# Optimization experiments

Measured on AMD Instinct MI355X. Metric: run time of the kernel, lower is better.

Reference implementation:

```python
import jax, jax.numpy as jnp
import numpy as np

B, L0, L1, NS, D, H, NL, HM = 16, 512, 256, 32, 256, 8, 4, 4
T = L0 + L1 + NS + 1
HD = D // H
EPS = 1e-5
SCALE = HD ** -0.5


def setup_inputs() -> dict:
    key = jax.random.key(0)
    ks = jax.random.split(key, 20)
    s = 0.02
    return {
        'seq_tokens_0': jax.random.normal(ks[0], (B, L0, D), jnp.float32),
        'seq_tokens_1': jax.random.normal(ks[1], (B, L1, D), jnp.float32),
        'seq_lens_0': jax.random.randint(ks[2], (B,), 0, L0),
        'seq_lens_1': jax.random.randint(ks[3], (B,), 0, L1),
        'ns_tokens': jax.random.normal(ks[4], (B, NS, D), jnp.float32),
        'domain_emb': jax.random.normal(ks[5], (2, D), jnp.float32) * s,
        'cls_token': jax.random.normal(ks[6], (1, 1, D), jnp.float32) * s,
        'ln1_w': jnp.ones((NL, D), jnp.float32),
        'ln1_b': jnp.zeros((NL, D), jnp.float32),
        'qkv_w': jax.random.normal(ks[7], (NL, D, 3 * D), jnp.float32) * s,
        'qkv_b': jnp.zeros((NL, 3 * D), jnp.float32),
        'out_w': jax.random.normal(ks[8], (NL, D, D), jnp.float32) * s,
        'out_b': jnp.zeros((NL, D), jnp.float32),
        'ln2_w': jnp.ones((NL, D), jnp.float32),
        'ln2_b': jnp.zeros((NL, D), jnp.float32),
        'ffn1_w': jax.random.normal(ks[9], (NL, D, HM * D), jnp.float32) * s,
        'ffn1_b': jnp.zeros((NL, HM * D), jnp.float32),
        'ffn2_w': jax.random.normal(ks[10], (NL, HM * D, D), jnp.float32) * s,
        'ffn2_b': jnp.zeros((NL, D), jnp.float32),
        'fln_w': jnp.ones((D,), jnp.float32),
        'fln_b': jnp.zeros((D,), jnp.float32),
    }


def _ln(x, w, b):
    m = jnp.mean(x, -1, keepdims=True)
    v = jnp.var(x, -1, keepdims=True)
    return (x - m) * jax.lax.rsqrt(v + EPS) * w + b


def _build_mask(seq_lens_0, seq_lens_1):
    # static block structure: intra-domain causal, S<->NS bidirectional, CLS sink row
    base = jnp.zeros((T, T), bool)
    base = base.at[:L0, :L0].set(jnp.tril(jnp.ones((L0, L0), bool)))
    base = base.at[L0:L0 + L1, L0:L0 + L1].set(jnp.tril(jnp.ones((L1, L1), bool)))
    ns_s, ns_e = L0 + L1, L0 + L1 + NS
    base = base.at[:ns_s, ns_s:ns_e].set(True)   # S -> NS
    base = base.at[ns_s:ns_e, :ns_e].set(True)   # NS -> S and NS -> NS
    base = base.at[T - 1, :ns_e].set(True)       # CLS reads all S/NS
    base = base.at[T - 1, T - 1].set(True)       # CLS reads itself
    # per-batch padding mask on keys of each seq segment
    kv = jnp.ones((B, T), bool)
    kv = kv.at[:, :L0].set(jnp.arange(L0)[None, :] < seq_lens_0[:, None])
    kv = kv.at[:, L0:L0 + L1].set(jnp.arange(L1)[None, :] < seq_lens_1[:, None])
    return base[None] & kv[:, None, :]  # [B, T, T]


def _attention(x, mask, qkv_w, qkv_b, out_w, out_b):
    qkv = (x @ qkv_w + qkv_b).reshape(B, T, 3, H, HD)
    q, k, v = qkv[:, :, 0], qkv[:, :, 1], qkv[:, :, 2]
    scores = jnp.einsum('bqhd,bkhd->bhqk', q, k) * SCALE
    m = mask[:, None]  # [B,1,T,T]
    s = jnp.where(m, scores, -jnp.inf)
    any_valid = jnp.any(m, -1, keepdims=True)
    mx = jnp.where(any_valid, jnp.max(s, -1, keepdims=True), 0.0)
    e = jnp.exp(s - mx)  # masked entries exp(-inf)=0
    denom = jnp.sum(e, -1, keepdims=True)
    probs = e / jnp.maximum(denom, 1e-30)  # fully-masked rows -> zeros
    out = jnp.einsum('bhqk,bkhd->bqhd', probs, v).reshape(B, T, D)
    return out @ out_w + out_b


def reference(seq_tokens_0, seq_tokens_1, seq_lens_0, seq_lens_1, ns_tokens,
              domain_emb, cls_token, ln1_w, ln1_b, qkv_w, qkv_b, out_w, out_b,
              ln2_w, ln2_b, ffn1_w, ffn1_b, ffn2_w, ffn2_b, fln_w, fln_b):
    t0 = seq_tokens_0 + domain_emb[0][None, None, :]
    t1 = seq_tokens_1 + domain_emb[1][None, None, :]
    cls = jnp.broadcast_to(cls_token, (B, 1, D))
    x = jnp.concatenate([t0, t1, ns_tokens, cls], axis=1)  # [B,T,D]
    mask = _build_mask(seq_lens_0, seq_lens_1)
    for l in range(NL):
        x = x + _attention(_ln(x, ln1_w[l], ln1_b[l]), mask,
                           qkv_w[l], qkv_b[l], out_w[l], out_b[l])
        h = _ln(x, ln2_w[l], ln2_b[l])
        h = jax.nn.gelu(h @ ffn1_w[l] + ffn1_b[l], approximate=False)
        x = x + h @ ffn2_w[l] + ffn2_b[l]
    x = _ln(x, fln_w, fln_b)
    return x[:, -1, :]  # CLS state [B,D]
```

## Files before the change

kernel.cpp:

```cpp
#include <hip/hip_runtime.h>
#include <hip/hip_bf16.h>
#include <math.h>

typedef __attribute__((ext_vector_type(8))) unsigned short ushort8;
typedef __attribute__((ext_vector_type(8))) short short8;
typedef __attribute__((ext_vector_type(4))) float f32x4;
typedef __attribute__((ext_vector_type(4))) unsigned short ushort4v;
typedef __attribute__((ext_vector_type(4))) int i32x4;
typedef unsigned int u32;

namespace {
constexpr int B = 16, L0 = 512, L1 = 256, NS = 32, D = 256, H = 8, NL = 4, HM = 4;
constexpr int T = L0 + L1 + NS + 1;
constexpr int HD = D / H;
constexpr int NS_S = L0 + L1;
constexpr int TPAD = 832;
constexpr int ROWP = 13312;
constexpr float EPS = 1e-5f;
constexpr float SCL2  = 0.17677669529663687f * 1.4426950408889634f;
}

__device__ __forceinline__ ushort f2bf(float f) {
    union { float f; unsigned u; } v; v.f = f;
    return (ushort)((v.u + 0x7fffu + ((v.u >> 16) & 1u)) >> 16);
}

__device__ __forceinline__ u32 cvtpk(float a, float b) {
    u32 r;
    asm("v_cvt_pk_bf16_f32 %0, %1, %2" : "=v"(r) : "v"(a), "v"(b));
    return r;
}

__device__ __forceinline__ void gload_lds16(const void* g, void* l) {
    __builtin_amdgcn_global_load_lds(
        (const __attribute__((address_space(1))) u32*)g,
        (__attribute__((address_space(3))) u32*)l, 16, 0, 0);
}

__global__ __launch_bounds__(256) void k_idx(
    const int* __restrict__ len0, const int* __restrict__ len1,
    int* __restrict__ offs, int* __restrict__ rowinfo)
{
    __shared__ int so[17];
    const int tid = threadIdx.x;
    if (tid == 0) {
        int acc = 0;
        for (int b = 0; b < 16; ++b) {
            so[b] = acc;
            const int nv = len0[b] + len1[b] + 33;
            acc += ((nv + 63) >> 6) << 6;
        }
        so[16] = acc;
    }
    __syncthreads();
    if (tid < 17) offs[tid] = so[tid];
    for (int r = tid; r < ROWP; r += 256) {
        int info = -1;
        if (r < so[16]) {
            int b = 15;
            for (int j = 0; j < 15; ++j) if (r < so[j + 1]) { b = j; break; }
            const int loc = r - so[b];
            const int n0 = len0[b], n1 = len1[b];
            if (loc < n0 + n1 + 33) {
                const int t = (loc < n0) ? loc
                            : (loc < n0 + n1) ? (L0 + loc - n0)
                            : (NS_S + loc - n0 - n1);
                info = (b << 16) | t;
            }
        }
        rowinfo[r] = info;
    }
}

__global__ __launch_bounds__(256) void k_wprep_all(
    const float* __restrict__ qkvw, const float* __restrict__ outw,
    const float* __restrict__ f1w, const float* __restrict__ f2w,
    ushort* __restrict__ qkvt, ushort* __restrict__ outt,
    ushort* __restrict__ f1t, ushort* __restrict__ f2t)
{
    int id = blockIdx.x;
    const float* src; ushort* dst; int K, N;
    if (id < 768)        { src = qkvw; dst = qkvt; K = 256;  N = 768;  }
    else if (id < 1024)  { id -= 768;  src = outw; dst = outt; K = 256; N = 256; }
    else if (id < 2048)  { id -= 1024; src = f1w;  dst = f1t;  K = 256; N = 1024; }
    else                 { id -= 2048; src = f2w;  dst = f2t;  K = 1024; N = 256; }
    const int ktiles = K >> 5, per = ktiles * (N >> 5);
    const int layer = id / per, rem = id % per;
    const int kb = (rem % ktiles) * 32, nb = (rem / ktiles) * 32;
    src += (size_t)layer * K * N; dst += (size_t)layer * K * N;

    __shared__ float t[32][33];
    const int c = threadIdx.x & 31, r8 = threadIdx.x >> 5;
#pragma unroll
    for (int rr = 0; rr < 32; rr += 8)
        t[r8 + rr][c] = src[(size_t)(kb + r8 + rr) * N + nb + c];
    __syncthreads();
#pragma unroll
    for (int rr = 0; rr < 32; rr += 8)
        dst[(size_t)(nb + r8 + rr) * K + kb + c] = f2bf(t[c][r8 + rr]);
}

__global__ __launch_bounds__(256) void k_build_ln(
    const float* __restrict__ s0, const float* __restrict__ s1,
    const float* __restrict__ ns, const float* __restrict__ dom,
    const float* __restrict__ cls, const float* __restrict__ lnw,
    const float* __restrict__ lnb, const int* __restrict__ rowinfo,
    float* __restrict__ x, ushort* __restrict__ xn)
{
    const int wid = threadIdx.x >> 6, lane = threadIdx.x & 63;
    const int row = blockIdx.x * 4 + wid;
    if (row >= ROWP) return;
    const int d0 = lane * 4;
    const int info = rowinfo[row];
    if (info < 0) {
        float4 z = {0.f, 0.f, 0.f, 0.f};
        *(float4*)(x + (size_t)row * D + d0) = z;
        ushort4v z4 = {0, 0, 0, 0};
        *(ushort4v*)(xn + (size_t)row * D + d0) = z4;
        return;
    }
    const int b = info >> 16, t = info & 0xFFFF;
    float4 v;
    if (t < L0) {
        v = *(const float4*)(s0 + ((size_t)b * L0 + t) * D + d0);
        float4 dm = *(const float4*)(dom + d0);
        v.x += dm.x; v.y += dm.y; v.z += dm.z; v.w += dm.w;
    } else if (t < NS_S) {
        v = *(const float4*)(s1 + ((size_t)b * L1 + (t - L0)) * D + d0);
        float4 dm = *(const float4*)(dom + D + d0);
        v.x += dm.x; v.y += dm.y; v.z += dm.z; v.w += dm.w;
    } else if (t < NS_S + NS) {
        v = *(const float4*)(ns + ((size_t)b * NS + (t - NS_S)) * D + d0);
    } else {
        v = *(const float4*)(cls + d0);
    }
    *(float4*)(x + (size_t)row * D + d0) = v;
    float s  = v.x + v.y + v.z + v.w;
    float ss = v.x * v.x + v.y * v.y + v.z * v.z + v.w * v.w;
#pragma unroll
    for (int o = 32; o; o >>= 1) { s += __shfl_xor(s, o); ss += __shfl_xor(ss, o); }
    const float mean = s * (1.f / D);
    const float var  = ss * (1.f / D) - mean * mean;
    const float r = rsqrtf(var + EPS);
    float4 wv = *(const float4*)(lnw + d0);
    float4 bv = *(const float4*)(lnb + d0);
    ushort4v o4;
    o4[0] = f2bf((v.x - mean) * r * wv.x + bv.x);
    o4[1] = f2bf((v.y - mean) * r * wv.y + bv.y);
    o4[2] = f2bf((v.z - mean) * r * wv.z + bv.z);
    o4[3] = f2bf((v.w - mean) * r * wv.w + bv.w);
    *(ushort4v*)(xn + (size_t)row * D + d0) = o4;
}

template<bool GELU, bool OBF, bool CLSW>
__global__ __launch_bounds__(256) void k_gemm_mfma(
    const ushort* __restrict__ A, const ushort* __restrict__ Wt,
    const float* __restrict__ bias, void* __restrict__ Cout,
    const int* __restrict__ offs, const int* __restrict__ len0,
    const int* __restrict__ len1, int N, int K, int nOff)
{
    __shared__ ushort As[2][128 * 64];
    __shared__ ushort Bs[2][128 * 64];
    const int tid = threadIdx.x;
    const int lane = tid & 63, w = tid >> 6;
    const int lo = lane & 15, g = lane >> 4;
    const int wr = w >> 1, wc = w & 1;
    int m0;
    if (CLSW) {
        const int bb = blockIdx.x;
        const int clsrow = offs[bb] + len0[bb] + len1[bb] + 32;
        m0 = (clsrow >> 7) << 7;
    } else {
        m0 = blockIdx.x * 128;
        if (m0 >= offs[16]) return;
    }
    const int n0 = (blockIdx.y + nOff) * 128;

    f32x4 zero = {0.f, 0.f, 0.f, 0.f};
    f32x4 acc[4][4];
#pragma unroll
    for (int mi = 0; mi < 4; ++mi)
#pragma unroll
        for (int ni = 0; ni < 4; ++ni) acc[mi][ni] = zero;

    const ushort* srcA[4];
    const ushort* srcB[4];
    int ldsOff[4];
#pragma unroll
    for (int i = 0; i < 4; ++i) {
        const int idx16 = (w * 4 + i) * 64 + lane;
        const int row = idx16 >> 3;
        const int scb = ((idx16 & 7) * 16) ^ ((row & 7) << 4);
        srcA[i] = A  + (size_t)(m0 + row) * K + (scb >> 1);
        srcB[i] = Wt + (size_t)(n0 + row) * K + (scb >> 1);
        ldsOff[i] = (w * 4 + i) * 512;
    }

    const int NT = K >> 6;
#pragma unroll
    for (int i = 0; i < 4; ++i) {
        gload_lds16(srcA[i], &As[0][ldsOff[i]]);
        gload_lds16(srcB[i], &Bs[0][ldsOff[i]]);
    }
    asm volatile("s_waitcnt vmcnt(0)");
    __syncthreads();

    for (int t = 0; t < NT; ++t) {
        const int buf = t & 1;
        if (t + 1 < NT) {
            const int nb = buf ^ 1, ko = (t + 1) * 64;
#pragma unroll
            for (int i = 0; i < 4; ++i) {
                gload_lds16(srcA[i] + ko, &As[nb][ldsOff[i]]);
                gload_lds16(srcB[i] + ko, &Bs[nb][ldsOff[i]]);
            }
        }
#pragma unroll
        for (int kk = 0; kk < 2; ++kk) {
            const int kb = (kk * 64 + g * 16) ^ ((lo & 7) << 4);
            short8 af[4], bfr[4];
#pragma unroll
            for (int mi = 0; mi < 4; ++mi)
                af[mi] = *(const short8*)&As[buf][(wr * 64 + mi * 16 + lo) * 64 + (kb >> 1)];
#pragma unroll
            for (int ni = 0; ni < 4; ++ni)
                bfr[ni] = *(const short8*)&Bs[buf][(wc * 64 + ni * 16 + lo) * 64 + (kb >> 1)];
#pragma unroll
            for (int mi = 0; mi < 4; ++mi)
#pragma unroll
                for (int ni = 0; ni < 4; ++ni)
                    acc[mi][ni] = __builtin_amdgcn_mfma_f32_16x16x32_bf16(
                        af[mi], bfr[ni], acc[mi][ni], 0, 0, 0);
        }
        asm volatile("s_waitcnt vmcnt(0)");
        __syncthreads();
    }

    float bv[4];
#pragma unroll
    for (int ni = 0; ni < 4; ++ni) bv[ni] = bias[n0 + wc * 64 + ni * 16 + lo];
#pragma unroll
    for (int mi = 0; mi < 4; ++mi) {
#pragma unroll
        for (int i = 0; i < 4; ++i) {
            const int row = m0 + wr * 64 + mi * 16 + g * 4 + i;
#pragma unroll
            for (int ni = 0; ni < 4; ++ni) {
                const int col = n0 + wc * 64 + ni * 16 + lo;
                float v = acc[mi][ni][i] + bv[ni];
                if (GELU) v = 0.5f * v * (1.0f + erff(v * 0.70710678118654752f));
                if (OBF) ((ushort*)Cout)[(size_t)row * N + col] = f2bf(v);
                else     ((float*)Cout)[(size_t)row * N + col] = v;
            }
        }
    }
}

template<int MODE, bool CLSW>
__global__ __launch_bounds__(256) void k_gemm_fused(
    const ushort* __restrict__ A, const ushort* __restrict__ Wt,
    const float* __restrict__ bias, const float* __restrict__ res,
    const float* __restrict__ lnw, const float* __restrict__ lnb,
    float* __restrict__ xout, ushort* __restrict__ xnout,
    float* __restrict__ dout, const int* __restrict__ offs,
    const int* __restrict__ rowinfo, const int* __restrict__ len0,
    const int* __restrict__ len1, int K)
{
    __shared__ ushort As[2][64 * 64];
    __shared__ ushort Bs[2][256 * 64];
    __shared__ float redS[64][4];
    __shared__ float redQ[64][4];
    const int tid = threadIdx.x;
    const int lane = tid & 63, w = tid >> 6;
    const int lo = lane & 15, g = lane >> 4;
    int m0;
    if (CLSW) {
        const int bb = blockIdx.x;
        const int clsrow = offs[bb] + len0[bb] + len1[bb] + 32;
        m0 = (clsrow >> 6) << 6;
    } else {
        m0 = blockIdx.x * 64;
        if (m0 >= offs[16]) return;
    }

    f32x4 zero = {0.f, 0.f, 0.f, 0.f};
    f32x4 acc[4][4];
#pragma unroll
    for (int mi = 0; mi < 4; ++mi)
#pragma unroll
        for (int ni = 0; ni < 4; ++ni) acc[mi][ni] = zero;

    const ushort* srcA[2]; int ldsOffA[2];
    const ushort* srcB[8]; int ldsOffB[8];
#pragma unroll
    for (int j = 0; j < 2; ++j) {
        const int idx16 = j * 256 + tid;
        const int row = idx16 >> 3;
        const int scb = ((idx16 & 7) * 16) ^ ((row & 7) << 4);
        srcA[j] = A + (size_t)(m0 + row) * K + (scb >> 1);
        ldsOffA[j] = idx16 * 8;
    }
#pragma unroll
    for (int j = 0; j < 8; ++j) {
        const int idx16 = j * 256 + tid;
        const int row = idx16 >> 3;
        const int scb = ((idx16 & 7) * 16) ^ ((row & 7) << 4);
        srcB[j] = Wt + (size_t)row * K + (scb >> 1);
        ldsOffB[j] = idx16 * 8;
    }

    const int NT = K >> 6;
#pragma unroll
    for (int j = 0; j < 2; ++j) gload_lds16(srcA[j], &As[0][ldsOffA[j]]);
#pragma unroll
    for (int j = 0; j < 8; ++j) gload_lds16(srcB[j], &Bs[0][ldsOffB[j]]);
    asm volatile("s_waitcnt vmcnt(0)");
    __syncthreads();

    for (int t = 0; t < NT; ++t) {
        const int buf = t & 1;
        if (t + 1 < NT) {
            const int nb = buf ^ 1, ko = (t + 1) * 64;
#pragma unroll
            for (int j = 0; j < 2; ++j) gload_lds16(srcA[j] + ko, &As[nb][ldsOffA[j]]);
#pragma unroll
            for (int j = 0; j < 8; ++j) gload_lds16(srcB[j] + ko, &Bs[nb][ldsOffB[j]]);
        }
#pragma unroll
        for (int kk = 0; kk < 2; ++kk) {
            const int kb = (kk * 64 + g * 16) ^ ((lo & 7) << 4);
            short8 af[4], bfr[4];
#pragma unroll
            for (int mi = 0; mi < 4; ++mi)
                af[mi] = *(const short8*)&As[buf][(mi * 16 + lo) * 64 + (kb >> 1)];
#pragma unroll
            for (int ni = 0; ni < 4; ++ni)
                bfr[ni] = *(const short8*)&Bs[buf][(w * 64 + ni * 16 + lo) * 64 + (kb >> 1)];
#pragma unroll
            for (int mi = 0; mi < 4; ++mi)
#pragma unroll
                for (int ni = 0; ni < 4; ++ni)
                    acc[mi][ni] = __builtin_amdgcn_mfma_f32_16x16x32_bf16(
                        af[mi], bfr[ni], acc[mi][ni], 0, 0, 0);
        }
        asm volatile("s_waitcnt vmcnt(0)");
        __syncthreads();
    }

    float bv[4], lw[4], lb[4];
#pragma unroll
    for (int ni = 0; ni < 4; ++ni) {
        const int c = w * 64 + ni * 16 + lo;
        bv[ni] = bias[c]; lw[ni] = lnw[c]; lb[ni] = lnb[c];
    }
#pragma unroll
    for (int mi = 0; mi < 4; ++mi) {
#pragma unroll
        for (int i = 0; i < 4; ++i) {
            const int r64 = mi * 16 + g * 4 + i;
            const int row = m0 + r64;
            float s = 0.f, q = 0.f;
#pragma unroll
            for (int ni = 0; ni < 4; ++ni) {
                const int col = w * 64 + ni * 16 + lo;
                float v = acc[mi][ni][i] + bv[ni] + res[(size_t)row * 256 + col];
                acc[mi][ni][i] = v;
                s += v; q += v * v;
            }
            s += __shfl_xor(s, 1); q += __shfl_xor(q, 1);
            s += __shfl_xor(s, 2); q += __shfl_xor(q, 2);
            s += __shfl_xor(s, 4); q += __shfl_xor(q, 4);
            s += __shfl_xor(s, 8); q += __shfl_xor(q, 8);
            if (lo == 0) { redS[r64][w] = s; redQ[r64][w] = q; }
        }
    }
    __syncthreads();
#pragma unroll
    for (int mi = 0; mi < 4; ++mi) {
#pragma unroll
        for (int i = 0; i < 4; ++i) {
            const int r64 = mi * 16 + g * 4 + i;
            const int row = m0 + r64;
            const float S = redS[r64][0] + redS[r64][1] + redS[r64][2] + redS[r64][3];
            const float Q = redQ[r64][0] + redQ[r64][1] + redQ[r64][2] + redQ[r64][3];
            const float mean = S * (1.f / 256.f);
            const float var  = Q * (1.f / 256.f) - mean * mean;
            const float rstd = rsqrtf(var + EPS);
            if (MODE == 0) {
#pragma unroll
                for (int ni = 0; ni < 4; ++ni) {
                    const int col = w * 64 + ni * 16 + lo;
                    const float v = acc[mi][ni][i];
                    xout[(size_t)row * 256 + col] = v;
                    xnout[(size_t)row * 256 + col] = f2bf((v - mean) * rstd * lw[ni] + lb[ni]);
                }
            } else {
                const int info = rowinfo[row];
                if (info >= 0 && (info & 0xFFFF) == T - 1) {
                    const int bq = info >> 16;
#pragma unroll
                    for (int ni = 0; ni < 4; ++ni) {
                        const int col = w * 64 + ni * 16 + lo;
                        dout[(size_t)bq * 256 + col] =
                            (acc[mi][ni][i] - mean) * rstd * lw[ni] + lb[ni];
                    }
                }
            }
        }
    }
}

__global__ __launch_bounds__(256) void k_repack(
    const ushort* __restrict__ qkv, ushort* __restrict__ Kb, ushort* __restrict__ Vt,
    const int* __restrict__ offs, const int* __restrict__ len0,
    const int* __restrict__ len1)
{
    const int bh = blockIdx.x, tt = blockIdx.y;
    const int b = bh >> 3, h = bh & 7;
    const int nv = len0[b] + len1[b] + 33;
    const int t0 = tt * 64;
    if (t0 >= nv) return;
    const int base = offs[b];
    const int tid = threadIdx.x;
    const int r = tid >> 2, c = tid & 3;
    __shared__ ushort vtile[64][40];
    const ushort* kp = qkv + (size_t)(base + t0 + r) * 768 + 256 + h * HD + c * 8;
    ushort8 k8 = *(const ushort8*)kp;
    ushort8 v8 = *(const ushort8*)(kp + 256);
    *(ushort8*)(Kb + ((size_t)bh * TPAD + t0 + r) * HD + c * 8) = k8;
    *(ushort8*)&vtile[r][c * 8] = v8;
    __syncthreads();
    const int d = tid >> 3, cc = tid & 7;
    ushort8 o;
#pragma unroll
    for (int j = 0; j < 8; ++j) o[j] = vtile[cc * 8 + j][d];
    *(ushort8*)(Vt + ((size_t)bh * HD + d) * TPAD + t0 + cc * 8) = o;
}

template<bool CLSONLY>
__global__ __launch_bounds__(256) void k_flash(
    const ushort* __restrict__ qkv, const ushort* __restrict__ Kb,
    const ushort* __restrict__ Vt, const int* __restrict__ offs,
    const int* __restrict__ len0, const int* __restrict__ len1,
    ushort* __restrict__ out)
{
    const int bh = blockIdx.x;
    const int b = bh >> 3, h = bh & 7;
    const int clen0 = len0[b], cns = clen0 + len1[b];
    const int nv = cns + 33;
    const int tl = (nv - 1) >> 6, tn0 = cns >> 6;
    int qt;
    if (CLSONLY) qt = tl;
    else { qt = 12 - (int)blockIdx.y; if (qt > tl) return; }

    const int base = offs[b];
    const int tid = threadIdx.x, lane = tid & 63, w = tid >> 6;
    const int lo = lane & 15, g = lane >> 4;
    const int b4 = g & 1, b5 = g >> 1;
    const int q0t = qt * 64;
    const int q = q0t + w * 16 + lo;

    short8 qf = *(const short8*)(qkv + (size_t)(base + q) * 768 + h * HD + g * 8);

    const ushort* Kbase = Kb + (size_t)bh * TPAD * HD;
    const ushort* Vbase = Vt + (size_t)bh * HD * TPAD;

    f32x4 acc0 = {0.f, 0.f, 0.f, 0.f}, acc1 = {0.f, 0.f, 0.f, 0.f};
    float mrow = -1e30f, srow = 0.f;

    const int kts = (q0t >= clen0 && (q0t + 63) < cns) ? (clen0 >> 6) : 0;
    const int nc = qt - kts + 1;
    const int estart = (qt + 1 > tn0) ? (qt + 1) : tn0;
    const int extra = (tl >= estart) ? (tl - estart + 1) : 0;
    const int ntiles = nc + extra;
    auto ktile = [&](int it) { return (it < nc) ? (kts + it) : (estart + (it - nc)); };

    auto maskrow = [&](int k0, int n, const f32x4& sn, float pv[4], float& tmax) {
#pragma unroll
        for (int i = 0; i < 4; ++i) {
            const int k = k0 + n * 16 + g * 4 + i;
            const bool win = (k >= cns) & (k < cns + 32);
            bool m;
            if (q < clen0)         m = (k <= q) | win;
            else if (q < cns)      m = ((k >= clen0) & (k <= q)) | win;
            else if (q < cns + 32) m = (k < cns + 32);
            else                   m = (k < cns + 32) | (k == q);
            const float sv = m ? sn[i] * SCL2 : -1e30f;
            pv[i] = sv;
            tmax = fmaxf(tmax, sv);
        }
    };
    auto xpose = [&](const u32 C0[4], const u32 C1[4], short8& pb0, short8& pb1) {
        u32 pb0u[4], pb1u[4];
#pragma unroll
        for (int n = 0; n < 4; ++n) {
            const u32 F0 = (u32)__shfl_xor((int)C0[n], 16);
            const u32 F1 = (u32)__shfl_xor((int)C1[n], 16);
            const u32 G00 = b4 ? F0 : C0[n];
            const u32 G01 = b4 ? C0[n] : F0;
            const u32 G10 = b4 ? F1 : C1[n];
            const u32 G11 = b4 ? C1[n] : F1;
            const u32 H00 = (u32)__shfl_xor((int)G00, 32);
            const u32 H01 = (u32)__shfl_xor((int)G01, 32);
            const u32 H10 = (u32)__shfl_xor((int)G10, 32);
            const u32 H11 = (u32)__shfl_xor((int)G11, 32);
            const bool keep = (b5 == b4);
            const u32 S00 = keep ? G00 : H00;
            const u32 S01 = keep ? G01 : H01;
            const u32 S10 = keep ? G10 : H10;
            const u32 S11 = keep ? G11 : H11;
            const bool take = (b5 == (n & 1));
            if ((n >> 1) == 0) {
                pb0u[0] = take ? S00 : pb0u[0];
                pb0u[1] = take ? S10 : pb0u[1];
                pb0u[2] = take ? S01 : pb0u[2];
                pb0u[3] = take ? S11 : pb0u[3];
            } else {
                pb1u[0] = take ? S00 : pb1u[0];
                pb1u[1] = take ? S10 : pb1u[1];
                pb1u[2] = take ? S01 : pb1u[2];
                pb1u[3] = take ? S11 : pb1u[3];
            }
        }
        i32x4 t0 = { (int)pb0u[0], (int)pb0u[1], (int)pb0u[2], (int)pb0u[3] };
        i32x4 t1 = { (int)pb1u[0], (int)pb1u[1], (int)pb1u[2], (int)pb1u[3] };
        pb0 = __builtin_bit_cast(short8, t0);
        pb1 = __builtin_bit_cast(short8, t1);
    };

    for (int it = 0; it < ntiles; ) {
        const bool has2 = (it + 1 < ntiles);
        const int kA = ktile(it) * 64;
        const int kB = has2 ? ktile(it + 1) * 64 : kA;

        short8 kfA[4], kfB[4];
#pragma unroll
        for (int n = 0; n < 4; ++n)
            kfA[n] = *(const short8*)(Kbase + (size_t)(kA + n * 16 + lo) * HD + g * 8);
        if (has2) {
#pragma unroll
            for (int n = 0; n < 4; ++n)
                kfB[n] = *(const short8*)(Kbase + (size_t)(kB + n * 16 + lo) * HD + g * 8);
        }

        const ushort* VA = Vbase + kA;
        short8 a00 = *(const short8*)(VA + (size_t)lo * TPAD + g * 8);
        short8 a01 = *(const short8*)(VA + (size_t)lo * TPAD + 32 + g * 8);
        short8 a10 = *(const short8*)(VA + (size_t)(16 + lo) * TPAD + g * 8);
        short8 a11 = *(const short8*)(VA + (size_t)(16 + lo) * TPAD + 32 + g * 8);
        short8 e00, e01, e10, e11;
        if (has2) {
            const ushort* VB = Vbase + kB;
            e00 = *(const short8*)(VB + (size_t)lo * TPAD + g * 8);
            e01 = *(const short8*)(VB + (size_t)lo * TPAD + 32 + g * 8);
            e10 = *(const short8*)(VB + (size_t)(16 + lo) * TPAD + g * 8);
            e11 = *(const short8*)(VB + (size_t)(16 + lo) * TPAD + 32 + g * 8);
        }

        float pvA[4][4], pvB[4][4];
        float tmax = -1e30f;
#pragma unroll
        for (int n = 0; n < 4; ++n) {
            f32x4 z = {0.f, 0.f, 0.f, 0.f};
            f32x4 sn = __builtin_amdgcn_mfma_f32_16x16x32_bf16(kfA[n], qf, z, 0, 0, 0);
            maskrow(kA, n, sn, pvA[n], tmax);
        }
        if (has2) {
#pragma unroll
            for (int n = 0; n < 4; ++n) {
                f32x4 z = {0.f, 0.f, 0.f, 0.f};
                f32x4 sn = __builtin_amdgcn_mfma_f32_16x16x32_bf16(kfB[n], qf, z, 0, 0, 0);
                maskrow(kB, n, sn, pvB[n], tmax);
            }
        }

        tmax = fmaxf(tmax, __shfl_xor(tmax, 16));
        tmax = fmaxf(tmax, __shfl_xor(tmax, 32));
        const float mnew = fmaxf(mrow, tmax);
        if (mnew > mrow) {
            const float scl = exp2f(mrow - mnew);
            srow *= scl;
#pragma unroll
            for (int i = 0; i < 4; ++i) { acc0[i] *= scl; acc1[i] *= scl; }
            mrow = mnew;
        }

        u32 CA0[4], CA1[4], CB0[4], CB1[4];
        float psum = 0.f;
#pragma unroll
        for (int n = 0; n < 4; ++n) {
            float e0 = (pvA[n][0] > -1e29f) ? exp2f(pvA[n][0] - mrow) : 0.f;
            float e1 = (pvA[n][1] > -1e29f) ? exp2f(pvA[n][1] - mrow) : 0.f;
            float e2 = (pvA[n][2] > -1e29f) ? exp2f(pvA[n][2] - mrow) : 0.f;
            float e3 = (pvA[n][3] > -1e29f) ? exp2f(pvA[n][3] - mrow) : 0.f;
            psum += (e0 + e1) + (e2 + e3);
            CA0[n] = cvtpk(e0, e1);
            CA1[n] = cvtpk(e2, e3);
        }
        if (has2) {
#pragma unroll
            for (int n = 0; n < 4; ++n) {
                float e0 = (pvB[n][0] > -1e29f) ? exp2f(pvB[n][0] - mrow) : 0.f;
                float e1 = (pvB[n][1] > -1e29f) ? exp2f(pvB[n][1] - mrow) : 0.f;
                float e2 = (pvB[n][2] > -1e29f) ? exp2f(pvB[n][2] - mrow) : 0.f;
                float e3 = (pvB[n][3] > -1e29f) ? exp2f(pvB[n][3] - mrow) : 0.f;
                psum += (e0 + e1) + (e2 + e3);
                CB0[n] = cvtpk(e0, e1);
                CB1[n] = cvtpk(e2, e3);
            }
        }
        psum += __shfl_xor(psum, 16);
        psum += __shfl_xor(psum, 32);
        srow += psum;

        short8 pb0, pb1;
        xpose(CA0, CA1, pb0, pb1);
        acc0 = __builtin_amdgcn_mfma_f32_16x16x32_bf16(a00, pb0, acc0, 0, 0, 0);
        acc0 = __builtin_amdgcn_mfma_f32_16x16x32_bf16(a01, pb1, acc0, 0, 0, 0);
        acc1 = __builtin_amdgcn_mfma_f32_16x16x32_bf16(a10, pb0, acc1, 0, 0, 0);
        acc1 = __builtin_amdgcn_mfma_f32_16x16x32_bf16(a11, pb1, acc1, 0, 0, 0);
        if (has2) {
            xpose(CB0, CB1, pb0, pb1);
            acc0 = __builtin_amdgcn_mfma_f32_16x16x32_bf16(e00, pb0, acc0, 0, 0, 0);
            acc0 = __builtin_amdgcn_mfma_f32_16x16x32_bf16(e01, pb1, acc0, 0, 0, 0);
            acc1 = __builtin_amdgcn_mfma_f32_16x16x32_bf16(e10, pb0, acc1, 0, 0, 0);
            acc1 = __builtin_amdgcn_mfma_f32_16x16x32_bf16(e11, pb1, acc1, 0, 0, 0);
        }

        it += has2 ? 2 : 1;
    }

    if (q < nv) {
        const float inv = 1.f / fmaxf(srow, 1e-30f);
        ushort* orow = out + (size_t)(base + q) * D + h * HD;
        *(u32*)(orow + g * 4)          = cvtpk(acc0[0] * inv, acc0[1] * inv);
        *(u32*)(orow + g * 4 + 2)      = cvtpk(acc0[2] * inv, acc0[3] * inv);
        *(u32*)(orow + 16 + g * 4)     = cvtpk(acc1[0] * inv, acc1[1] * inv);
        *(u32*)(orow + 16 + g * 4 + 2) = cvtpk(acc1[2] * inv, acc1[3] * inv);
    }
}

extern "C" void kernel_launch(void* const* d_in, const int* in_sizes, int n_in,
                              void* d_out, int out_size, void* d_ws, size_t ws_size,
                              hipStream_t stream)
{
    const float* seq0 = (const float*)d_in[0];
    const float* seq1 = (const float*)d_in[1];
    const int*   len0 = (const int*)d_in[2];
    const int*   len1 = (const int*)d_in[3];
    const float* nst  = (const float*)d_in[4];
    const float* dom  = (const float*)d_in[5];
    const float* cls  = (const float*)d_in[6];
    const float* ln1w = (const float*)d_in[7];
    const float* ln1b = (const float*)d_in[8];
    const float* qkvw = (const float*)d_in[9];
    const float* qkvb = (const float*)d_in[10];
    const float* outw = (const float*)d_in[11];
    const float* outb = (const float*)d_in[12];
    const float* ln2w = (const float*)d_in[13];
    const float* ln2b = (const float*)d_in[14];
    const float* f1w  = (const float*)d_in[15];
    const float* f1b  = (const float*)d_in[16];
    const float* f2w  = (const float*)d_in[17];
    const float* f2b  = (const float*)d_in[18];
    const float* flnw = (const float*)d_in[19];
    const float* flnb = (const float*)d_in[20];

    float*  x   = (float*)d_ws;
    ushort* xn  = (ushort*)(x + (size_t)ROWP * D);
    ushort* big = xn + (size_t)ROWP * D;
    ushort* Kb  = big + (size_t)ROWP * HM * D;
    ushort* Vt  = Kb + (size_t)B * H * TPAD * HD;
    ushort* qkvw_t = Vt + (size_t)B * H * TPAD * HD;
    ushort* outw_t = qkvw_t + (size_t)NL * 768 * 256;
    ushort* f1w_t  = outw_t + (size_t)NL * 256 * 256;
    ushort* f2w_t  = f1w_t  + (size_t)NL * 1024 * 256;
    int* offs      = (int*)(f2w_t + (size_t)NL * 256 * 1024);
    int* rowinfo   = offs + 32;

    k_wprep_all<<<3072, 256, 0, stream>>>(qkvw, outw, f1w, f2w,
                                          qkvw_t, outw_t, f1w_t, f2w_t);
    k_idx<<<1, 256, 0, stream>>>(len0, len1, offs, rowinfo);
    k_build_ln<<<ROWP / 4, 256, 0, stream>>>(seq0, seq1, nst, dom, cls,
                                             ln1w, ln1b, rowinfo, x, xn);

    const int gmm = ROWP / 128;
    const int gf  = ROWP / 64;

    for (int l = 0; l < NL; ++l) {
        const bool last = (l == NL - 1);
        if (!last) {
            k_gemm_mfma<false, true, false><<<dim3(gmm, 6), 256, 0, stream>>>(
                xn, qkvw_t + (size_t)l * 768 * 256, qkvb + (size_t)l * 3 * D, big,
                offs, len0, len1, 3 * D, D, 0);
        } else {
            k_gemm_mfma<false, true, false><<<dim3(gmm, 4), 256, 0, stream>>>(
                xn, qkvw_t + (size_t)l * 768 * 256, qkvb + (size_t)l * 3 * D, big,
                offs, len0, len1, 3 * D, D, 2);
            k_gemm_mfma<false, true, true><<<dim3(B, 2), 256, 0, stream>>>(
                xn, qkvw_t + (size_t)l * 768 * 256, qkvb + (size_t)l * 3 * D, big,
                offs, len0, len1, 3 * D, D, 0);
        }
        k_repack<<<dim3(B * H, 13), 256, 0, stream>>>(big, Kb, Vt, offs, len0, len1);
        if (!last)
            k_flash<false><<<dim3(B * H, 13), 256, 0, stream>>>(
                big, Kb, Vt, offs, len0, len1, xn);
        else
            k_flash<true><<<dim3(B * H, 1), 256, 0, stream>>>(
                big, Kb, Vt, offs, len0, len1, xn);
        if (!last)
            k_gemm_fused<0, false><<<gf, 256, 0, stream>>>(
                xn, outw_t + (size_t)l * 256 * 256, outb + (size_t)l * D, x,
                ln2w + l * D, ln2b + l * D, x, xn, nullptr, offs, rowinfo,
                len0, len1, D);
        else
            k_gemm_fused<0, true><<<B, 256, 0, stream>>>(
                xn, outw_t + (size_t)l * 256 * 256, outb + (size_t)l * D, x,
                ln2w + l * D, ln2b + l * D, x, xn, nullptr, offs, rowinfo,
                len0, len1, D);
        if (!last)
            k_gemm_mfma<true, true, false><<<dim3(gmm, 8), 256, 0, stream>>>(
                xn, f1w_t + (size_t)l * 1024 * 256, f1b + (size_t)l * HM * D, big,
                offs, len0, len1, HM * D, D, 0);
        else
            k_gemm_mfma<true, true, true><<<dim3(B, 8), 256, 0, stream>>>(
                xn, f1w_t + (size_t)l * 1024 * 256, f1b + (size_t)l * HM * D, big,
                offs, len0, len1, HM * D, D, 0);
        if (!last)
            k_gemm_fused<0, false><<<gf, 256, 0, stream>>>(
                big, f2w_t + (size_t)l * 256 * 1024, f2b + (size_t)l * D, x,
                ln1w + (l + 1) * D, ln1b + (l + 1) * D, x, xn, nullptr, offs,
                rowinfo, len0, len1, HM * D);
        else
            k_gemm_fused<1, true><<<B, 256, 0, stream>>>(
                big, f2w_t + (size_t)l * 256 * 1024, f2b + (size_t)l * D, x,
                flnw, flnb, nullptr, nullptr, (float*)d_out, offs, rowinfo,
                len0, len1, HM * D);
    }
}
```

Before: 465.1 us.

## Drop index kernel, split flash into per-wave blocks, skip masks on interior tiles

Removes the k_idx kernel and the offs/rowinfo arrays, so every kernel recomputes batch offsets inline from the sequence lengths. The flash attention kernel now launches one 64-thread block per 16-query wave (grid z=4), giving finer scheduling and per-wave tile ranges. Its inner loop goes from two K tiles per iteration to one, software-prefetches the next K tile, and skips per-element mask evaluation on fully unmasked interior tiles. This trades a launch and some global reads for redundant scalar offset loops in each block, and the single-tile loop exposes less instruction-level parallelism.

```diff
diff --git a/kernel.cpp b/kernel.cpp
--- a/kernel.cpp
+++ b/kernel.cpp
@@ -37,39 +37,11 @@
         (__attribute__((address_space(3))) u32*)l, 16, 0, 0);
 }
 
-__global__ __launch_bounds__(256) void k_idx(
-    const int* __restrict__ len0, const int* __restrict__ len1,
-    int* __restrict__ offs, int* __restrict__ rowinfo)
-{
-    __shared__ int so[17];
-    const int tid = threadIdx.x;
-    if (tid == 0) {
-        int acc = 0;
-        for (int b = 0; b < 16; ++b) {
-            so[b] = acc;
-            const int nv = len0[b] + len1[b] + 33;
-            acc += ((nv + 63) >> 6) << 6;
-        }
-        so[16] = acc;
-    }
-    __syncthreads();
-    if (tid < 17) offs[tid] = so[tid];
-    for (int r = tid; r < ROWP; r += 256) {
-        int info = -1;
-        if (r < so[16]) {
-            int b = 15;
-            for (int j = 0; j < 15; ++j) if (r < so[j + 1]) { b = j; break; }
-            const int loc = r - so[b];
-            const int n0 = len0[b], n1 = len1[b];
-            if (loc < n0 + n1 + 33) {
-                const int t = (loc < n0) ? loc
-                            : (loc < n0 + n1) ? (L0 + loc - n0)
-                            : (NS_S + loc - n0 - n1);
-                info = (b << 16) | t;
-            }
-        }
-        rowinfo[r] = info;
-    }
+__device__ __forceinline__ int offs_of(const int* __restrict__ l0,
+                                       const int* __restrict__ l1, int b) {
+    int acc = 0;
+    for (int j = 0; j < b; ++j) acc += ((l0[j] + l1[j] + 96) >> 6) << 6;
+    return acc;
 }
 
 __global__ __launch_bounds__(256) void k_wprep_all(
@@ -104,22 +76,38 @@
     const float* __restrict__ s0, const float* __restrict__ s1,
     const float* __restrict__ ns, const float* __restrict__ dom,
     const float* __restrict__ cls, const float* __restrict__ lnw,
-    const float* __restrict__ lnb, const int* __restrict__ rowinfo,
-    float* __restrict__ x, ushort* __restrict__ xn)
+    const float* __restrict__ lnb, const int* __restrict__ len0,
+    const int* __restrict__ len1, float* __restrict__ x, ushort* __restrict__ xn)
 {
     const int wid = threadIdx.x >> 6, lane = threadIdx.x & 63;
     const int row = blockIdx.x * 4 + wid;
     if (row >= ROWP) return;
     const int d0 = lane * 4;
-    const int info = rowinfo[row];
-    if (info < 0) {
+
+    int bsel = -1, t = -1, acc = 0;
+    for (int j = 0; j < 16; ++j) {
+        const int n0 = len0[j], n1 = len1[j];
+        const int nvj = n0 + n1 + 33;
+        const int cap = ((nvj + 63) >> 6) << 6;
+        if (row < acc + cap) {
+            const int loc = row - acc;
+            if (loc < nvj)
+                t = (loc < n0) ? loc
+                  : (loc < n0 + n1) ? (L0 + loc - n0)
+                  : (NS_S + loc - n0 - n1);
+            bsel = j;
+            break;
+        }
+        acc += cap;
+    }
+    if (bsel < 0 || t < 0) {
         float4 z = {0.f, 0.f, 0.f, 0.f};
         *(float4*)(x + (size_t)row * D + d0) = z;
         ushort4v z4 = {0, 0, 0, 0};
         *(ushort4v*)(xn + (size_t)row * D + d0) = z4;
         return;
     }
-    const int b = info >> 16, t = info & 0xFFFF;
+    const int b = bsel;
     float4 v;
     if (t < L0) {
         v = *(const float4*)(s0 + ((size_t)b * L0 + t) * D + d0);
@@ -156,8 +144,8 @@
 __global__ __launch_bounds__(256) void k_gemm_mfma(
     const ushort* __restrict__ A, const ushort* __restrict__ Wt,
     const float* __restrict__ bias, void* __restrict__ Cout,
-    const int* __restrict__ offs, const int* __restrict__ len0,
-    const int* __restrict__ len1, int N, int K, int nOff)
+    const int* __restrict__ len0, const int* __restrict__ len1,
+    int N, int K, int nOff)
 {
     __shared__ ushort As[2][128 * 64];
     __shared__ ushort Bs[2][128 * 64];
@@ -168,11 +156,11 @@
     int m0;
     if (CLSW) {
         const int bb = blockIdx.x;
-        const int clsrow = offs[bb] + len0[bb] + len1[bb] + 32;
+        const int clsrow = offs_of(len0, len1, bb) + len0[bb] + len1[bb] + 32;
         m0 = (clsrow >> 7) << 7;
     } else {
         m0 = blockIdx.x * 128;
-        if (m0 >= offs[16]) return;
+        if (m0 >= offs_of(len0, len1, 16)) return;
     }
     const int n0 = (blockIdx.y + nOff) * 128;
 
@@ -262,8 +250,7 @@
     const float* __restrict__ bias, const float* __restrict__ res,
     const float* __restrict__ lnw, const float* __restrict__ lnb,
     float* __restrict__ xout, ushort* __restrict__ xnout,
-    float* __restrict__ dout, const int* __restrict__ offs,
-    const int* __restrict__ rowinfo, const int* __restrict__ len0,
+    float* __restrict__ dout, const int* __restrict__ len0,
     const int* __restrict__ len1, int K)
 {
     __shared__ ushort As[2][64 * 64];
@@ -273,14 +260,14 @@
     const int tid = threadIdx.x;
     const int lane = tid & 63, w = tid >> 6;
     const int lo = lane & 15, g = lane >> 4;
-    int m0;
+    int m0, clsrow = -1, bb = 0;
     if (CLSW) {
-        const int bb = blockIdx.x;
-        const int clsrow = offs[bb] + len0[bb] + len1[bb] + 32;
+        bb = blockIdx.x;
+        clsrow = offs_of(len0, len1, bb) + len0[bb] + len1[bb] + 32;
         m0 = (clsrow >> 6) << 6;
     } else {
         m0 = blockIdx.x * 64;
-        if (m0 >= offs[16]) return;
+        if (m0 >= offs_of(len0, len1, 16)) return;
     }
 
     f32x4 zero = {0.f, 0.f, 0.f, 0.f};
@@ -395,13 +382,11 @@
                     xnout[(size_t)row * 256 + col] = f2bf((v - mean) * rstd * lw[ni] + lb[ni]);
                 }
             } else {
-                const int info = rowinfo[row];
-                if (info >= 0 && (info & 0xFFFF) == T - 1) {
-                    const int bq = info >> 16;
+                if (row == clsrow) {
 #pragma unroll
                     for (int ni = 0; ni < 4; ++ni) {
                         const int col = w * 64 + ni * 16 + lo;
-                        dout[(size_t)bq * 256 + col] =
+                        dout[(size_t)bb * 256 + col] =
                             (acc[mi][ni][i] - mean) * rstd * lw[ni] + lb[ni];
                     }
                 }
@@ -412,15 +397,14 @@
 
 __global__ __launch_bounds__(256) void k_repack(
     const ushort* __restrict__ qkv, ushort* __restrict__ Kb, ushort* __restrict__ Vt,
-    const int* __restrict__ offs, const int* __restrict__ len0,
-    const int* __restrict__ len1)
+    const int* __restrict__ len0, const int* __restrict__ len1)
 {
     const int bh = blockIdx.x, tt = blockIdx.y;
     const int b = bh >> 3, h = bh & 7;
     const int nv = len0[b] + len1[b] + 33;
     const int t0 = tt * 64;
     if (t0 >= nv) return;
-    const int base = offs[b];
+    const int base = offs_of(len0, len1, b);
     const int tid = threadIdx.x;
     const int r = tid >> 2, c = tid & 3;
     __shared__ ushort vtile[64][40];
@@ -438,11 +422,10 @@
 }
 
 template<bool CLSONLY>
-__global__ __launch_bounds__(256) void k_flash(
+__global__ __launch_bounds__(64) void k_flash(
     const ushort* __restrict__ qkv, const ushort* __restrict__ Kb,
-    const ushort* __restrict__ Vt, const int* __restrict__ offs,
-    const int* __restrict__ len0, const int* __restrict__ len1,
-    ushort* __restrict__ out)
+    const ushort* __restrict__ Vt, const int* __restrict__ len0,
+    const int* __restrict__ len1, ushort* __restrict__ out)
 {
     const int bh = blockIdx.x;
     const int b = bh >> 3, h = bh & 7;
@@ -453,12 +436,14 @@
     if (CLSONLY) qt = tl;
     else { qt = 12 - (int)blockIdx.y; if (qt > tl) return; }
 
-    const int base = offs[b];
-    const int tid = threadIdx.x, lane = tid & 63, w = tid >> 6;
+    const int base = offs_of(len0, len1, b);
+    const int w = blockIdx.z;
+    const int lane = threadIdx.x;
     const int lo = lane & 15, g = lane >> 4;
     const int b4 = g & 1, b5 = g >> 1;
     const int q0t = qt * 64;
-    const int q = q0t + w * 16 + lo;
+    const int qmin = q0t + w * 16, qmax = qmin + 15;
+    const int q = qmin + lo;
 
     short8 qf = *(const short8*)(qkv + (size_t)(base + q) * 768 + h * HD + g * 8);
 
@@ -468,28 +453,13 @@
     f32x4 acc0 = {0.f, 0.f, 0.f, 0.f}, acc1 = {0.f, 0.f, 0.f, 0.f};
     float mrow = -1e30f, srow = 0.f;
 
-    const int kts = (q0t >= clen0 && (q0t + 63) < cns) ? (clen0 >> 6) : 0;
+    const int kts = (qmin >= clen0 && qmax < cns) ? (clen0 >> 6) : 0;
     const int nc = qt - kts + 1;
     const int estart = (qt + 1 > tn0) ? (qt + 1) : tn0;
     const int extra = (tl >= estart) ? (tl - estart + 1) : 0;
     const int ntiles = nc + extra;
     auto ktile = [&](int it) { return (it < nc) ? (kts + it) : (estart + (it - nc)); };
 
-    auto maskrow = [&](int k0, int n, const f32x4& sn, float pv[4], float& tmax) {
-#pragma unroll
-        for (int i = 0; i < 4; ++i) {
-            const int k = k0 + n * 16 + g * 4 + i;
-            const bool win = (k >= cns) & (k < cns + 32);
-            bool m;
-            if (q < clen0)         m = (k <= q) | win;
-            else if (q < cns)      m = ((k >= clen0) & (k <= q)) | win;
-            else if (q < cns + 32) m = (k < cns + 32);
-            else                   m = (k < cns + 32) | (k == q);
-            const float sv = m ? sn[i] * SCL2 : -1e30f;
-            pv[i] = sv;
-            tmax = fmaxf(tmax, sv);
-        }
-    };
     auto xpose = [&](const u32 C0[4], const u32 C1[4], short8& pb0, short8& pb1) {
         u32 pb0u[4], pb1u[4];
 #pragma unroll
@@ -528,50 +498,63 @@
         pb1 = __builtin_bit_cast(short8, t1);
     };
 
-    for (int it = 0; it < ntiles; ) {
-        const bool has2 = (it + 1 < ntiles);
-        const int kA = ktile(it) * 64;
-        const int kB = has2 ? ktile(it + 1) * 64 : kA;
-
-        short8 kfA[4], kfB[4];
+    short8 kf[4];
+    {
+        const int k0 = ktile(0) * 64;
 #pragma unroll
         for (int n = 0; n < 4; ++n)
-            kfA[n] = *(const short8*)(Kbase + (size_t)(kA + n * 16 + lo) * HD + g * 8);
-        if (has2) {
-#pragma unroll
-            for (int n = 0; n < 4; ++n)
-                kfB[n] = *(const short8*)(Kbase + (size_t)(kB + n * 16 + lo) * HD + g * 8);
-        }
-
-        const ushort* VA = Vbase + kA;
-        short8 a00 = *(const short8*)(VA + (size_t)lo * TPAD + g * 8);
-        short8 a01 = *(const short8*)(VA + (size_t)lo * TPAD + 32 + g * 8);
-        short8 a10 = *(const short8*)(VA + (size_t)(16 + lo) * TPAD + g * 8);
-        short8 a11 = *(const short8*)(VA + (size_t)(16 + lo) * TPAD + 32 + g * 8);
-        short8 e00, e01, e10, e11;
-        if (has2) {
-            const ushort* VB = Vbase + kB;
-            e00 = *(const short8*)(VB + (size_t)lo * TPAD + g * 8);
-            e01 = *(const short8*)(VB + (size_t)lo * TPAD + 32 + g * 8);
-            e10 = *(const short8*)(VB + (size_t)(16 + lo) * TPAD + g * 8);
-            e11 = *(const short8*)(VB + (size_t)(16 + lo) * TPAD + 32 + g * 8);
-        }
-
-        float pvA[4][4], pvB[4][4];
+            kf[n] = *(const short8*)(Kbase + (size_t)(k0 + n * 16 + lo) * HD + g * 8);
+    }
+
+    for (int it = 0; it < ntiles; ++it) {
+        const int k0 = ktile(it) * 64;
+
+        const bool interior =
+            (qmax < clen0 && k0 + 63 <= qmin) ||
+            (qmin >= clen0 && qmax < cns && k0 >= clen0 && k0 + 63 <= qmin) ||
+            (qmin >= cns && k0 + 63 < cns + 32);
+
+        const ushort* V0 = Vbase + k0;
+        short8 a00 = *(const short8*)(V0 + (size_t)lo * TPAD + g * 8);
+        short8 a01 = *(const short8*)(V0 + (size_t)lo * TPAD + 32 + g * 8);
+        short8 a10 = *(const short8*)(V0 + (size_t)(16 + lo) * TPAD + g * 8);
+        short8 a11 = *(const short8*)(V0 + (size_t)(16 + lo) * TPAD + 32 + g * 8);
+
+        float pv[4][4];
         float tmax = -1e30f;
 #pragma unroll
         for (int n = 0; n < 4; ++n) {
             f32x4 z = {0.f, 0.f, 0.f, 0.f};
-            f32x4 sn = __builtin_amdgcn_mfma_f32_16x16x32_bf16(kfA[n], qf, z, 0, 0, 0);
-            maskrow(kA, n, sn, pvA[n], tmax);
-        }
-        if (has2) {
-#pragma unroll
-            for (int n = 0; n < 4; ++n) {
-                f32x4 z = {0.f, 0.f, 0.f, 0.f};
-                f32x4 sn = __builtin_amdgcn_mfma_f32_16x16x32_bf16(kfB[n], qf, z, 0, 0, 0);
-                maskrow(kB, n, sn, pvB[n], tmax);
+            f32x4 sn = __builtin_amdgcn_mfma_f32_16x16x32_bf16(kf[n], qf, z, 0, 0, 0);
+            if (interior) {
+#pragma unroll
+                for (int i = 0; i < 4; ++i) {
+                    pv[n][i] = sn[i] * SCL2;
+                    tmax = fmaxf(tmax, pv[n][i]);
+                }
+            } else {
+#pragma unroll
+                for (int i = 0; i < 4; ++i) {
+                    const int k = k0 + n * 16 + g * 4 + i;
+                    const bool win = (k >= cns) & (k < cns + 32);
+                    bool m;
+                    if (q < clen0)         m = (k <= q) | win;
+                    else if (q < cns)      m = ((k >= clen0) & (k <= q)) | win;
+                    else if (q < cns + 32) m = (k < cns + 32);
+                    else                   m = (k < cns + 32) | (k == q);
+                    const float sv = m ? sn[i] * SCL2 : -1e30f;
+                    pv[n][i] = sv;
+                    tmax = fmaxf(tmax, sv);
+                }
             }
+        }
+
+        short8 kf2[4];
+        if (it + 1 < ntiles) {
+            const int k1 = ktile(it + 1) * 64;
+#pragma unroll
+            for (int n = 0; n < 4; ++n)
+                kf2[n] = *(const short8*)(Kbase + (size_t)(k1 + n * 16 + lo) * HD + g * 8);
         }
 
         tmax = fmaxf(tmax, __shfl_xor(tmax, 16));
@@ -585,49 +568,31 @@
             mrow = mnew;
         }
 
-        u32 CA0[4], CA1[4], CB0[4], CB1[4];
+        u32 C0[4], C1[4];
         float psum = 0.f;
 #pragma unroll
         for (int n = 0; n < 4; ++n) {
-            float e0 = (pvA[n][0] > -1e29f) ? exp2f(pvA[n][0] - mrow) : 0.f;
-            float e1 = (pvA[n][1] > -1e29f) ? exp2f(pvA[n][1] - mrow) : 0.f;
-            float e2 = (pvA[n][2] > -1e29f) ? exp2f(pvA[n][2] - mrow) : 0.f;
-            float e3 = (pvA[n][3] > -1e29f) ? exp2f(pvA[n][3] - mrow) : 0.f;
+            float e0 = (pv[n][0] > -1e29f) ? exp2f(pv[n][0] - mrow) : 0.f;
+            float e1 = (pv[n][1] > -1e29f) ? exp2f(pv[n][1] - mrow) : 0.f;
+            float e2 = (pv[n][2] > -1e29f) ? exp2f(pv[n][2] - mrow) : 0.f;
+            float e3 = (pv[n][3] > -1e29f) ? exp2f(pv[n][3] - mrow) : 0.f;
             psum += (e0 + e1) + (e2 + e3);
-            CA0[n] = cvtpk(e0, e1);
-            CA1[n] = cvtpk(e2, e3);
-        }
-        if (has2) {
-#pragma unroll
-            for (int n = 0; n < 4; ++n) {
-                float e0 = (pvB[n][0] > -1e29f) ? exp2f(pvB[n][0] - mrow) : 0.f;
-                float e1 = (pvB[n][1] > -1e29f) ? exp2f(pvB[n][1] - mrow) : 0.f;
-                float e2 = (pvB[n][2] > -1e29f) ? exp2f(pvB[n][2] - mrow) : 0.f;
-                float e3 = (pvB[n][3] > -1e29f) ? exp2f(pvB[n][3] - mrow) : 0.f;
-                psum += (e0 + e1) + (e2 + e3);
-                CB0[n] = cvtpk(e0, e1);
-                CB1[n] = cvtpk(e2, e3);
-            }
+            C0[n] = cvtpk(e0, e1);
+            C1[n] = cvtpk(e2, e3);
         }
         psum += __shfl_xor(psum, 16);
         psum += __shfl_xor(psum, 32);
         srow += psum;
 
         short8 pb0, pb1;
-        xpose(CA0, CA1, pb0, pb1);
+        xpose(C0, C1, pb0, pb1);
         acc0 = __builtin_amdgcn_mfma_f32_16x16x32_bf16(a00, pb0, acc0, 0, 0, 0);
         acc0 = __builtin_amdgcn_mfma_f32_16x16x32_bf16(a01, pb1, acc0, 0, 0, 0);
         acc1 = __builtin_amdgcn_mfma_f32_16x16x32_bf16(a10, pb0, acc1, 0, 0, 0);
         acc1 = __builtin_amdgcn_mfma_f32_16x16x32_bf16(a11, pb1, acc1, 0, 0, 0);
-        if (has2) {
-            xpose(CB0, CB1, pb0, pb1);
-            acc0 = __builtin_amdgcn_mfma_f32_16x16x32_bf16(e00, pb0, acc0, 0, 0, 0);
-            acc0 = __builtin_amdgcn_mfma_f32_16x16x32_bf16(e01, pb1, acc0, 0, 0, 0);
-            acc1 = __builtin_amdgcn_mfma_f32_16x16x32_bf16(e10, pb0, acc1, 0, 0, 0);
-            acc1 = __builtin_amdgcn_mfma_f32_16x16x32_bf16(e11, pb1, acc1, 0, 0, 0);
-        }
-
-        it += has2 ? 2 : 1;
+
+#pragma unroll
+        for (int n = 0; n < 4; ++n) kf[n] = kf2[n];
     }
 
     if (q < nv) {
@@ -675,14 +640,11 @@
     ushort* outw_t = qkvw_t + (size_t)NL * 768 * 256;
     ushort* f1w_t  = outw_t + (size_t)NL * 256 * 256;
     ushort* f2w_t  = f1w_t  + (size_t)NL * 1024 * 256;
-    int* offs      = (int*)(f2w_t + (size_t)NL * 256 * 1024);
-    int* rowinfo   = offs + 32;
 
     k_wprep_all<<<3072, 256, 0, stream>>>(qkvw, outw, f1w, f2w,
                                           qkvw_t, outw_t, f1w_t, f2w_t);
-    k_idx<<<1, 256, 0, stream>>>(len0, len1, offs, rowinfo);
     k_build_ln<<<ROWP / 4, 256, 0, stream>>>(seq0, seq1, nst, dom, cls,
-                                             ln1w, ln1b, rowinfo, x, xn);
+                                             ln1w, ln1b, len0, len1, x, xn);
 
     const int gmm = ROWP / 128;
     const int gf  = ROWP / 64;
@@ -692,49 +654,46 @@
         if (!last) {
             k_gemm_mfma<false, true, false><<<dim3(gmm, 6), 256, 0, stream>>>(
                 xn, qkvw_t + (size_t)l * 768 * 256, qkvb + (size_t)l * 3 * D, big,
-                offs, len0, len1, 3 * D, D, 0);
+                len0, len1, 3 * D, D, 0);
         } else {
             k_gemm_mfma<false, true, false><<<dim3(gmm, 4), 256, 0, stream>>>(
                 xn, qkvw_t + (size_t)l * 768 * 256, qkvb + (size_t)l * 3 * D, big,
-                offs, len0, len1, 3 * D, D, 2);
+                len0, len1, 3 * D, D, 2);
             k_gemm_mfma<false, true, true><<<dim3(B, 2), 256, 0, stream>>>(
                 xn, qkvw_t + (size_t)l * 768 * 256, qkvb + (size_t)l * 3 * D, big,
-                offs, len0, len1, 3 * D, D, 0);
-        }
-        k_repack<<<dim3(B * H, 13), 256, 0, stream>>>(big, Kb, Vt, offs, len0, len1);
+                len0, len1, 3 * D, D, 0);
+        }
+        k_repack<<<dim3(B * H, 13), 256, 0, stream>>>(big, Kb, Vt, len0, len1);
         if (!last)
-            k_flash<false><<<dim3(B * H, 13), 256, 0, stream>>>(
-                big, Kb, Vt, offs, len0, len1, xn);
+            k_flash<false><<<dim3(B * H, 13, 4), 64, 0, stream>>>(
+                big, Kb, Vt, len0, len1, xn);
         else
-            k_flash<true><<<dim3(B * H, 1), 256, 0, stream>>>(
-                big, Kb, Vt, offs, len0, len1, xn);
+            k_flash<true><<<dim3(B * H, 1, 4), 64, 0, stream>>>(
+                big, Kb, Vt, len0, len1, xn);
         if (!last)
             k_gemm_fused<0, false><<<gf, 256, 0, stream>>>(
                 xn, outw_t + (size_t)l * 256 * 256, outb + (size_t)l * D, x,
-                ln2w + l * D, ln2b + l * D, x, xn, nullptr, offs, rowinfo,
-                len0, len1, D);
+                ln2w + l * D, ln2b + l * D, x, xn, nullptr, len0, len1, D);
         else
             k_gemm_fused<0, true><<<B, 256, 0, stream>>>(
                 xn, outw_t + (size_t)l * 256 * 256, outb + (size_t)l * D, x,
-                ln2w + l * D, ln2b + l * D, x, xn, nullptr, offs, rowinfo,
-                len0, len1, D);
+                ln2w + l * D, ln2b + l * D, x, xn, nullptr, len0, len1, D);
         if (!last)
             k_gemm_mfma<true, true, false><<<dim3(gmm, 8), 256, 0, stream>>>(
                 xn, f1w_t + (size_t)l * 1024 * 256, f1b + (size_t)l * HM * D, big,
-                offs, len0, len1, HM * D, D, 0);
+                len0, len1, HM * D, D, 0);
         else
             k_gemm_mfma<true, true, true><<<dim3(B, 8), 256, 0, stream>>>(
                 xn, f1w_t + (size_t)l * 1024 * 256, f1b + (size_t)l * HM * D, big,
-                offs, len0, len1, HM * D, D, 0);
+                len0, len1, HM * D, D, 0);
         if (!last)
             k_gemm_fused<0, false><<<gf, 256, 0, stream>>>(
                 big, f2w_t + (size_t)l * 256 * 1024, f2b + (size_t)l * D, x,
-                ln1w + (l + 1) * D, ln1b + (l + 1) * D, x, xn, nullptr, offs,
-                rowinfo, len0, len1, HM * D);
+                ln1w + (l + 1) * D, ln1b + (l + 1) * D, x, xn, nullptr,
+                len0, len1, HM * D);
         else
             k_gemm_fused<1, true><<<B, 256, 0, stream>>>(
                 big, f2w_t + (size_t)l * 256 * 1024, f2b + (size_t)l * D, x,
-                flnw, flnb, nullptr, nullptr, (float*)d_out, offs, rowinfo,
-                len0, len1, HM * D);
-    }
-}
+                flnw, flnb, nullptr, nullptr, (float*)d_out, len0, len1, HM * D);
+    }
+}
```

Result: no change. 458.4 us (median of 2 runs) (-1.4%).
